# Kernel optimization log

Measured on AMD Instinct MI355X. Metric: run time of the kernel, lower is better.

## Reference

```python
import jax, jax.numpy as jnp
import numpy as np

B, C, L, H, W = 2, 64, 8, 32, 32

def setup_inputs() -> dict:
    key = jax.random.key(0)
    ks = jax.random.split(key, 10)
    return {
        "q": jax.random.normal(ks[0], (B, C, L, H, W), dtype=jnp.float32),
        "k": jax.random.normal(ks[1], (B, C, L, H, W), dtype=jnp.float32),
        "v": jax.random.normal(ks[2], (B, C, L, H, W), dtype=jnp.float32),
        "wq": jax.random.normal(ks[3], (C,), dtype=jnp.float32) * 0.1,
        "bq": jax.random.normal(ks[4], (1,), dtype=jnp.float32) * 0.1,
        "wk": jax.random.normal(ks[5], (C,), dtype=jnp.float32) * 0.1,
        "bk": jax.random.normal(ks[6], (1,), dtype=jnp.float32) * 0.1,
        "wv": jax.random.normal(ks[7], (C, 3 * C), dtype=jnp.float32) * 0.1,
        "bv": jax.random.normal(ks[8], (C,), dtype=jnp.float32) * 0.1,
        "gamma_x": jax.random.normal(ks[9], (1,), dtype=jnp.float32) * 0.1,
    }


def reference(q, k, v, wq, bq, wk, bk, wv, bv, gamma_x):
    # q,k,v: [B,C,L,H,W]; 1x1x1 conv3d == channel contraction
    Bq, Cq, Lq, Hq, Wq = q.shape
    N = Lq * Hq * Wq
    qf = q.reshape(Bq, Cq, N)
    kf = k.reshape(Bq, Cq, N)
    vf = v.reshape(Bq, Cq, N)
    # query/key conv: C -> 1 channel => [B, N]
    pq = jnp.einsum('bcn,c->bn', qf, wq) + bq  # [B,N]
    pk = jnp.einsum('bcn,c->bn', kf, wk) + bk  # [B,N]
    # energy = bmm([B,N,1],[B,1,N]) = outer product -> [B,N,N]
    energy = pq[:, :, None] * pk[:, None, :]
    attn = jax.nn.softmax(energy, axis=-1)  # softmax over key index n
    # value path: cat(v, q, k) along channels -> [B,3C,N], then 3C -> C conv
    val = jnp.concatenate([vf, qf, kf], axis=1)
    pv = jnp.einsum('bdn,cd->bcn', val, wv) + bv[None, :, None]  # [B,C,N]
    # out[b,c,m] = sum_n pv[b,c,n] * attn[b,m,n]  (bmm with attn^T)
    out = jnp.einsum('bcn,bmn->bcm', pv, attn).reshape(Bq, Cq, Lq, Hq, Wq)
    return gamma_x * out + v
```

## Files before the change

kernel.cpp:

```cpp
#include <hip/hip_runtime.h>


typedef __attribute__((ext_vector_type(8))) __bf16 bf16x8;
typedef __attribute__((ext_vector_type(4))) float  f32x4;

#define NN 8192
#define CC 64
#define NJ 48

__global__ __launch_bounds__(256) void setup_kernel(
    const float* __restrict__ wv, float* __restrict__ wvT,
    float* __restrict__ G, float* __restrict__ T)
{
    int i0 = blockIdx.x * 256 + threadIdx.x;
    for (int i = i0; i < 2 * CC * NJ; i += 16 * 256) G[i] = 0.f;
    for (int i = i0; i < 2 * NJ; i += 16 * 256) T[i] = 0.f;
    for (int i = i0; i < 192 * 64; i += 16 * 256) {
        int d = i >> 6, c = i & 63;
        wvT[i] = wv[c * 192 + d];
    }
}

__global__ __launch_bounds__(512) void prep_kernel(
    const float* __restrict__ q, const float* __restrict__ k,
    const float* __restrict__ v,
    const float* __restrict__ wq, const float* __restrict__ bq,
    const float* __restrict__ wk, const float* __restrict__ bk,
    const float* __restrict__ wvT, const float* __restrict__ bv,
    float* __restrict__ pq, float* __restrict__ pk, __bf16* __restrict__ pvT)
{
    int t = threadIdx.x;
    int b  = blockIdx.x >> 7;
    int n0 = (blockIdx.x & 127) << 6;
    int n  = n0 + (t & 63);
    int cg = __builtin_amdgcn_readfirstlane(t >> 6);

    size_t bo = (size_t)b * CC * NN;
    float acc[8];
    #pragma unroll
    for (int j = 0; j < 8; j++) acc[j] = 0.f;
    float pqa = 0.f, pka = 0.f;

    {
        const float* sp = v + bo + n;
        const float* wp = wvT + cg * 8;
        #pragma unroll 8
        for (int dc = 0; dc < 64; dc++) {
            float x = sp[(size_t)dc * NN];
            #pragma unroll
            for (int j = 0; j < 8; j++) acc[j] = fmaf(x, wp[dc * 64 + j], acc[j]);
        }
    }
    {
        const float* sp = q + bo + n;
        const float* wp = wvT + 64 * 64 + cg * 8;
        #pragma unroll 8
        for (int dc = 0; dc < 64; dc++) {
            float x = sp[(size_t)dc * NN];
            #pragma unroll
            for (int j = 0; j < 8; j++) acc[j] = fmaf(x, wp[dc * 64 + j], acc[j]);
            if (cg == 0) pqa = fmaf(x, wq[dc], pqa);
        }
    }
    {
        const float* sp = k + bo + n;
        const float* wp = wvT + 128 * 64 + cg * 8;
        #pragma unroll 8
        for (int dc = 0; dc < 64; dc++) {
            float x = sp[(size_t)dc * NN];
            #pragma unroll
            for (int j = 0; j < 8; j++) acc[j] = fmaf(x, wp[dc * 64 + j], acc[j]);
            if (cg == 0) pka = fmaf(x, wk[dc], pka);
        }
    }

    #pragma unroll
    for (int j = 0; j < 8; j++) {
        int c = cg * 8 + j;
        pvT[((size_t)b * CC + c) * NN + n] = (__bf16)(acc[j] + bv[c]);
    }
    if (cg == 0) {
        pq[b * NN + n] = pqa + bq[0];
        pk[b * NN + n] = pka + bk[0];
    }
}

__global__ __launch_bounds__(256) void moment_kernel(
    const float* __restrict__ pk, const __bf16* __restrict__ pvT,
    float* __restrict__ G, float* __restrict__ T)
{
    __shared__ __align__(16) __bf16 pv_s[64][72];
    __shared__ __align__(16) __bf16 V_s[NJ][72];

    int t = threadIdx.x, lane = t & 63, wid = t >> 6;
    int quad = lane >> 4, cl = lane & 15;
    int b   = blockIdx.x >> 6;
    int nb0 = (blockIdx.x & 63) << 7;

    f32x4 acc[3];
    #pragma unroll
    for (int jt = 0; jt < 3; jt++) acc[jt] = (f32x4){0.f, 0.f, 0.f, 0.f};
    float tT[NJ / 48 * 48 ? 1 : 1];
    float tsum = 0.f;

    for (int s = 0; s < 2; s++) {
        int n0 = nb0 + s * 64;
        {
            int c = t >> 2, seg2 = (t & 3) << 1;
            const __bf16* gp = pvT + ((size_t)b * CC + c) * NN + n0;
            #pragma unroll
            for (int h = 0; h < 2; h++) {
                int seg = seg2 + h;
                *(bf16x8*)&pv_s[c][seg * 8] = *(const bf16x8*)(gp + seg * 8);
            }
        }
        {
            int n = t & 63, jg = t >> 6;
            float tv = pk[b * NN + n0 + n];
            float t2 = tv * tv, t4 = t2 * t2, t6 = t4 * t2, t12 = t6 * t6;
            float tp = 1.f;
            if (jg >= 1) tp = t12;
            if (jg >= 2) tp = t12 * t12;
            if (jg == 3) tp = t12 * t12 * t12;
            #pragma unroll
            for (int jj = 0; jj < 12; jj++) {
                V_s[jg * 12 + jj][n] = (__bf16)tp;
                tp *= tv;
            }
        }
        __syncthreads();

        #pragma unroll
        for (int k0 = 0; k0 < 64; k0 += 32) {
            bf16x8 a = *(const bf16x8*)&pv_s[wid * 16 + cl][k0 + quad * 8];
            #pragma unroll
            for (int jt = 0; jt < 3; jt++) {
                bf16x8 bf = *(const bf16x8*)&V_s[jt * 16 + cl][k0 + quad * 8];
                acc[jt] = __builtin_amdgcn_mfma_f32_16x16x32_bf16(a, bf, acc[jt], 0, 0, 0);
            }
        }
        if (t < NJ) {
            #pragma unroll
            for (int h = 0; h < 8; h++) {
                bf16x8 vv = *(const bf16x8*)&V_s[t][h * 8];
                #pragma unroll
                for (int e = 0; e < 8; e++) tsum += (float)vv[e];
            }
        }
        __syncthreads();
    }

    #pragma unroll
    for (int jt = 0; jt < 3; jt++)
        #pragma unroll
        for (int r = 0; r < 4; r++) {
            int c = wid * 16 + quad * 4 + r;
            int j = jt * 16 + cl;
            atomicAdd(&G[((size_t)b * CC + c) * NJ + j], acc[jt][r]);
        }
    if (t < NJ) atomicAdd(&T[b * NJ + t], tsum);
}

__global__ __launch_bounds__(256) void eval_kernel(
    const float* __restrict__ pq, const float* __restrict__ G,
    const float* __restrict__ T, const float* __restrict__ v,
    const float* __restrict__ gamma, float* __restrict__ out)
{
    int t = threadIdx.x;
    int b   = blockIdx.x >> 8;
    int mch = (blockIdx.x >> 3) & 31;
    int cg  = blockIdx.x & 7;

    int m = mch * 256 + t;
    float s = pq[b * NN + m];
    const float* Gr = G + ((size_t)b * CC + cg * 8) * NJ;
    const float* Tr = T + b * NJ;

    float acc[8];
    #pragma unroll
    for (int c = 0; c < 8; c++) acc[c] = 0.f;
    float z = 0.f, cj = 1.f;
    #pragma unroll
    for (int j = 0; j < NJ; j++) {
        if (j > 0) cj *= s * (1.0f / (float)j);
        z = fmaf(cj, Tr[j], z);
        #pragma unroll
        for (int c = 0; c < 8; c++) acc[c] = fmaf(cj, Gr[c * NJ + j], acc[c]);
    }
    float gz = gamma[0] / z;

    #pragma unroll
    for (int c = 0; c < 8; c++) {
        size_t idx = ((size_t)b * CC + cg * 8 + c) * NN + m;
        out[idx] = fmaf(gz, acc[c], v[idx]);
    }
}

extern "C" void kernel_launch(void* const* d_in, const int* in_sizes, int n_in,
                              void* d_out, int out_size, void* d_ws, size_t ws_size,
                              hipStream_t stream)
{
    const float* q     = (const float*)d_in[0];
    const float* k     = (const float*)d_in[1];
    const float* v     = (const float*)d_in[2];
    const float* wq    = (const float*)d_in[3];
    const float* bq    = (const float*)d_in[4];
    const float* wk    = (const float*)d_in[5];
    const float* bk    = (const float*)d_in[6];
    const float* wv    = (const float*)d_in[7];
    const float* bv    = (const float*)d_in[8];
    const float* gamma = (const float*)d_in[9];

    float*  pqw  = (float*)d_ws;
    float*  pkw  = pqw + 2 * NN;
    float*  wvT  = pkw + 2 * NN;
    float*  Gw   = wvT + 192 * 64;
    float*  Tw   = Gw + 2 * CC * NJ;
    __bf16* pvT  = (__bf16*)(Tw + 2 * NJ);

    setup_kernel<<<16, 256, 0, stream>>>(wv, wvT, Gw, Tw);
    prep_kernel<<<256, 512, 0, stream>>>(q, k, v, wq, bq, wk, bk, wvT, bv,
                                         pqw, pkw, pvT);
    moment_kernel<<<128, 256, 0, stream>>>(pkw, pvT, Gw, Tw);
    eval_kernel<<<512, 256, 0, stream>>>(pqw, Gw, Tw, v, gamma, (float*)d_out);
}
```

Baseline: 111.2 us.

## Fuse value projection into moment kernel using MFMA and drop pvT round trip

```diff
diff --git a/kernel.cpp b/kernel.cpp
--- a/kernel.cpp
+++ b/kernel.cpp
@@ -8,87 +8,35 @@
 #define CC 64
 #define NJ 48
 
-__global__ __launch_bounds__(256) void setup_kernel(
-    const float* __restrict__ wv, float* __restrict__ wvT,
-    float* __restrict__ G, float* __restrict__ T)
-{
-    int i0 = blockIdx.x * 256 + threadIdx.x;
-    for (int i = i0; i < 2 * CC * NJ; i += 16 * 256) G[i] = 0.f;
-    for (int i = i0; i < 2 * NJ; i += 16 * 256) T[i] = 0.f;
-    for (int i = i0; i < 192 * 64; i += 16 * 256) {
-        int d = i >> 6, c = i & 63;
-        wvT[i] = wv[c * 192 + d];
-    }
-}
-
-__global__ __launch_bounds__(512) void prep_kernel(
+__global__ __launch_bounds__(256) void pqpk_kernel(
     const float* __restrict__ q, const float* __restrict__ k,
-    const float* __restrict__ v,
     const float* __restrict__ wq, const float* __restrict__ bq,
     const float* __restrict__ wk, const float* __restrict__ bk,
-    const float* __restrict__ wvT, const float* __restrict__ bv,
-    float* __restrict__ pq, float* __restrict__ pk, __bf16* __restrict__ pvT)
-{
-    int t = threadIdx.x;
-    int b  = blockIdx.x >> 7;
-    int n0 = (blockIdx.x & 127) << 6;
-    int n  = n0 + (t & 63);
-    int cg = __builtin_amdgcn_readfirstlane(t >> 6);
-
-    size_t bo = (size_t)b * CC * NN;
-    float acc[8];
-    #pragma unroll
-    for (int j = 0; j < 8; j++) acc[j] = 0.f;
-    float pqa = 0.f, pka = 0.f;
-
-    {
-        const float* sp = v + bo + n;
-        const float* wp = wvT + cg * 8;
-        #pragma unroll 8
-        for (int dc = 0; dc < 64; dc++) {
-            float x = sp[(size_t)dc * NN];
-            #pragma unroll
-            for (int j = 0; j < 8; j++) acc[j] = fmaf(x, wp[dc * 64 + j], acc[j]);
-        }
-    }
-    {
-        const float* sp = q + bo + n;
-        const float* wp = wvT + 64 * 64 + cg * 8;
-        #pragma unroll 8
-        for (int dc = 0; dc < 64; dc++) {
-            float x = sp[(size_t)dc * NN];
-            #pragma unroll
-            for (int j = 0; j < 8; j++) acc[j] = fmaf(x, wp[dc * 64 + j], acc[j]);
-            if (cg == 0) pqa = fmaf(x, wq[dc], pqa);
-        }
-    }
-    {
-        const float* sp = k + bo + n;
-        const float* wp = wvT + 128 * 64 + cg * 8;
-        #pragma unroll 8
-        for (int dc = 0; dc < 64; dc++) {
-            float x = sp[(size_t)dc * NN];
-            #pragma unroll
-            for (int j = 0; j < 8; j++) acc[j] = fmaf(x, wp[dc * 64 + j], acc[j]);
-            if (cg == 0) pka = fmaf(x, wk[dc], pka);
-        }
-    }
-
-    #pragma unroll
-    for (int j = 0; j < 8; j++) {
-        int c = cg * 8 + j;
-        pvT[((size_t)b * CC + c) * NN + n] = (__bf16)(acc[j] + bv[c]);
-    }
-    if (cg == 0) {
-        pq[b * NN + n] = pqa + bq[0];
-        pk[b * NN + n] = pka + bk[0];
-    }
-}
-
-__global__ __launch_bounds__(256) void moment_kernel(
-    const float* __restrict__ pk, const __bf16* __restrict__ pvT,
+    float* __restrict__ pq, float* __restrict__ pk)
+{
+    int t = threadIdx.x, lane = t & 63, wid = t >> 6;
+    int b  = blockIdx.x >> 6;
+    int n  = ((blockIdx.x & 63) << 7) + ((wid & 1) << 6) + lane;
+
+    const float* src = (wid < 2) ? q : k;
+    const float* wgt = (wid < 2) ? wq : wk;
+    float bias       = (wid < 2) ? bq[0] : bk[0];
+    float* dst       = (wid < 2) ? pq : pk;
+
+    const float* sp = src + (size_t)b * CC * NN + n;
+    float a = 0.f;
+    #pragma unroll 8
+    for (int d = 0; d < 64; d++) a = fmaf(sp[(size_t)d * NN], wgt[d], a);
+    dst[b * NN + n] = a + bias;
+}
+
+__global__ __launch_bounds__(256) void fused_kernel(
+    const float* __restrict__ q, const float* __restrict__ k,
+    const float* __restrict__ v, const float* __restrict__ wv,
+    const float* __restrict__ bv, const float* __restrict__ pk,
     float* __restrict__ G, float* __restrict__ T)
 {
+    __shared__ __align__(16) __bf16 val_sT[64][200];
     __shared__ __align__(16) __bf16 pv_s[64][72];
     __shared__ __align__(16) __bf16 V_s[NJ][72];
 
@@ -96,47 +44,87 @@
     int quad = lane >> 4, cl = lane & 15;
     int b   = blockIdx.x >> 6;
     int nb0 = (blockIdx.x & 63) << 7;
-
-    f32x4 acc[3];
-    #pragma unroll
-    for (int jt = 0; jt < 3; jt++) acc[jt] = (f32x4){0.f, 0.f, 0.f, 0.f};
-    float tT[NJ / 48 * 48 ? 1 : 1];
+    size_t bo = (size_t)b * CC * NN;
+
+    bf16x8 wvA[6];
+    const float* wr = wv + (size_t)(wid * 16 + cl) * 192;
+    #pragma unroll
+    for (int ks = 0; ks < 6; ks++) {
+        f32x4 a0 = *(const f32x4*)(wr + ks * 32 + quad * 8);
+        f32x4 a1 = *(const f32x4*)(wr + ks * 32 + quad * 8 + 4);
+        #pragma unroll
+        for (int e = 0; e < 4; e++) {
+            wvA[ks][e]     = (__bf16)a0[e];
+            wvA[ks][4 + e] = (__bf16)a1[e];
+        }
+    }
+    float bvr[4];
+    #pragma unroll
+    for (int r = 0; r < 4; r++) bvr[r] = bv[wid * 16 + quad * 4 + r];
+
+    f32x4 accG[3];
+    #pragma unroll
+    for (int jt = 0; jt < 3; jt++) accG[jt] = (f32x4){0.f, 0.f, 0.f, 0.f};
     float tsum = 0.f;
 
     for (int s = 0; s < 2; s++) {
         int n0 = nb0 + s * 64;
-        {
-            int c = t >> 2, seg2 = (t & 3) << 1;
-            const __bf16* gp = pvT + ((size_t)b * CC + c) * NN + n0;
-            #pragma unroll
-            for (int h = 0; h < 2; h++) {
-                int seg = seg2 + h;
-                *(bf16x8*)&pv_s[c][seg * 8] = *(const bf16x8*)(gp + seg * 8);
-            }
-        }
-        {
-            int n = t & 63, jg = t >> 6;
-            float tv = pk[b * NN + n0 + n];
-            float t2 = tv * tv, t4 = t2 * t2, t6 = t4 * t2, t12 = t6 * t6;
+        if (wid < 3) {
+            int dt = t >> 3, no = t & 7;
+            int dbase = dt * 8;
+            const float* src = (dbase < 64)  ? (v + bo + (size_t)dbase * NN)
+                             : (dbase < 128) ? (q + bo + (size_t)(dbase - 64) * NN)
+                                             : (k + bo + (size_t)(dbase - 128) * NN);
+            float tile[8][8];
+            #pragma unroll
+            for (int dd = 0; dd < 8; dd++) {
+                f32x4 x0 = *(const f32x4*)(src + (size_t)dd * NN + n0 + no * 8);
+                f32x4 x1 = *(const f32x4*)(src + (size_t)dd * NN + n0 + no * 8 + 4);
+                #pragma unroll
+                for (int e = 0; e < 4; e++) { tile[dd][e] = x0[e]; tile[dd][4 + e] = x1[e]; }
+            }
+            #pragma unroll
+            for (int nn = 0; nn < 8; nn++) {
+                bf16x8 wb;
+                #pragma unroll
+                for (int dd = 0; dd < 8; dd++) wb[dd] = (__bf16)tile[dd][nn];
+                *(bf16x8*)&val_sT[no * 8 + nn][dbase] = wb;
+            }
+        } else {
+            float tv = pk[b * NN + n0 + lane];
             float tp = 1.f;
-            if (jg >= 1) tp = t12;
-            if (jg >= 2) tp = t12 * t12;
-            if (jg == 3) tp = t12 * t12 * t12;
-            #pragma unroll
-            for (int jj = 0; jj < 12; jj++) {
-                V_s[jg * 12 + jj][n] = (__bf16)tp;
+            #pragma unroll
+            for (int j = 0; j < NJ; j++) {
+                V_s[j][lane] = (__bf16)tp;
                 tp *= tv;
             }
         }
         __syncthreads();
+
+        f32x4 accP[4];
+        #pragma unroll
+        for (int nt = 0; nt < 4; nt++) accP[nt] = (f32x4){0.f, 0.f, 0.f, 0.f};
+        #pragma unroll
+        for (int ks = 0; ks < 6; ks++)
+            #pragma unroll
+            for (int nt = 0; nt < 4; nt++) {
+                bf16x8 bfr = *(const bf16x8*)&val_sT[nt * 16 + cl][ks * 32 + quad * 8];
+                accP[nt] = __builtin_amdgcn_mfma_f32_16x16x32_bf16(wvA[ks], bfr, accP[nt], 0, 0, 0);
+            }
+
+        #pragma unroll
+        for (int nt = 0; nt < 4; nt++)
+            #pragma unroll
+            for (int r = 0; r < 4; r++)
+                pv_s[wid * 16 + quad * 4 + r][nt * 16 + cl] = (__bf16)(accP[nt][r] + bvr[r]);
 
         #pragma unroll
         for (int k0 = 0; k0 < 64; k0 += 32) {
             bf16x8 a = *(const bf16x8*)&pv_s[wid * 16 + cl][k0 + quad * 8];
             #pragma unroll
             for (int jt = 0; jt < 3; jt++) {
-                bf16x8 bf = *(const bf16x8*)&V_s[jt * 16 + cl][k0 + quad * 8];
-                acc[jt] = __builtin_amdgcn_mfma_f32_16x16x32_bf16(a, bf, acc[jt], 0, 0, 0);
+                bf16x8 bfr = *(const bf16x8*)&V_s[jt * 16 + cl][k0 + quad * 8];
+                accG[jt] = __builtin_amdgcn_mfma_f32_16x16x32_bf16(a, bfr, accG[jt], 0, 0, 0);
             }
         }
         if (t < NJ) {
@@ -153,11 +141,9 @@
     #pragma unroll
     for (int jt = 0; jt < 3; jt++)
         #pragma unroll
-        for (int r = 0; r < 4; r++) {
-            int c = wid * 16 + quad * 4 + r;
-            int j = jt * 16 + cl;
-            atomicAdd(&G[((size_t)b * CC + c) * NJ + j], acc[jt][r]);
-        }
+        for (int r = 0; r < 4; r++)
+            atomicAdd(&G[((size_t)b * CC + wid * 16 + quad * 4 + r) * NJ + jt * 16 + cl],
+                      accG[jt][r]);
     if (t < NJ) atomicAdd(&T[b * NJ + t], tsum);
 }
 
@@ -211,16 +197,13 @@
     const float* bv    = (const float*)d_in[8];
     const float* gamma = (const float*)d_in[9];
 
-    float*  pqw  = (float*)d_ws;
-    float*  pkw  = pqw + 2 * NN;
-    float*  wvT  = pkw + 2 * NN;
-    float*  Gw   = wvT + 192 * 64;
-    float*  Tw   = Gw + 2 * CC * NJ;
-    __bf16* pvT  = (__bf16*)(Tw + 2 * NJ);
-
-    setup_kernel<<<16, 256, 0, stream>>>(wv, wvT, Gw, Tw);
-    prep_kernel<<<256, 512, 0, stream>>>(q, k, v, wq, bq, wk, bk, wvT, bv,
-                                         pqw, pkw, pvT);
-    moment_kernel<<<128, 256, 0, stream>>>(pkw, pvT, Gw, Tw);
+    float* pqw = (float*)d_ws;
+    float* pkw = pqw + 2 * NN;
+    float* Gw  = pkw + 2 * NN;
+    float* Tw  = Gw + 2 * CC * NJ;
+
+    hipMemsetAsync(Gw, 0, (2 * CC * NJ + 2 * NJ) * sizeof(float), stream);
+    pqpk_kernel<<<128, 256, 0, stream>>>(q, k, wq, bq, wk, bk, pqw, pkw);
+    fused_kernel<<<128, 256, 0, stream>>>(q, k, v, wv, bv, pkw, Gw, Tw);
     eval_kernel<<<512, 256, 0, stream>>>(pqw, Gw, Tw, v, gamma, (float*)d_out);
 }
```

Measured after the change: 98.50 us. -11.4%, faster.
